# Kernel optimization log

Hardware: AMD Instinct MI355X
Metric: run time of the kernel (lower is better)

## Reference

```python
import jax, jax.numpy as jnp
import numpy as np

B, IN, N, K = 8192, 1024, 4096, 409
BN_EPS = 1e-5
BOOST_STRENGTH = 1.0


def setup_inputs() -> dict:
    key = jax.random.key(0)
    k1, k2, k3, k4, k5 = jax.random.split(key, 5)
    x = jax.random.normal(k1, (B, IN), dtype=jnp.float32)
    W = jax.random.normal(k2, (N, IN), dtype=jnp.float32) * 0.03
    b = jax.random.normal(k3, (N,), dtype=jnp.float32) * 0.01
    wmask = jax.random.randint(k4, (N, IN), 0, 2, dtype=jnp.int32)
    dutyCycle = jax.random.uniform(k5, (N,), dtype=jnp.float32) * (K / N) * 2.0
    return {"x": x, "W": W, "b": b, "wmask": wmask, "dutyCycle": dutyCycle, "k": K}


def reference(x, W, b, wmask, dutyCycle, k):
    n = W.shape[0]
    # rezeroWeights: enforce fixed weight sparsity pattern
    Wm = W * wmask.astype(W.dtype)
    # Linear
    y = jnp.einsum("bi,ni->bn", x, Wm) + b
    # BatchNorm1d(affine=False), training mode: batch mean / biased variance
    mean = jnp.mean(y, axis=0)
    var = jnp.mean(jnp.square(y - mean), axis=0)
    y = (y - mean) / jnp.sqrt(var + BN_EPS)
    # KWinners with duty-cycle boosting (k < n path)
    targetDensity = jnp.float32(k) / n
    boostFactors = jnp.exp((targetDensity - dutyCycle) * BOOST_STRENGTH)
    boosted = jax.lax.stop_gradient(y) * boostFactors  # [B, n]
    _, idx = jax.lax.top_k(boosted, k)                 # [B, k]
    rows = jnp.arange(y.shape[0])[:, None]
    out = jnp.zeros_like(y).at[rows, idx].set(jnp.take_along_axis(y, idx, axis=1))
    return out
```

## Files before the change

### kernel.cpp

```cpp
#include <hip/hip_runtime.h>

#define BATCH 8192
#define INF   1024
#define NF    4096
#define BN_EPS 1e-5
#define NT    32

typedef __attribute__((ext_vector_type(8))) short short8v;
typedef __attribute__((ext_vector_type(4))) float f32x4;

#define FENCE asm volatile("" ::: "memory")
#define BARRIER do { FENCE; __builtin_amdgcn_s_barrier(); FENCE; } while (0)

__global__ void zero_ws(double* __restrict__ p) {
    p[blockIdx.x * 256 + threadIdx.x] = 0.0;
}

__device__ __forceinline__ void split3(float x, ushort& h0, ushort& h1, ushort& h2) {
    const unsigned u0 = __float_as_uint(x) & 0xFFFF0000u;
    const float    r1 = x - __uint_as_float(u0);
    const unsigned u1 = __float_as_uint(r1) & 0xFFFF0000u;
    const float    r2 = r1 - __uint_as_float(u1);
    h0 = (ushort)(u0 >> 16);
    h1 = (ushort)(u1 >> 16);
    h2 = (ushort)(__float_as_uint(r2) >> 16);
}

__global__ __launch_bounds__(256) void split_x_kernel(
    const float* __restrict__ X, ushort* __restrict__ xs)
{
    const size_t base = ((size_t)blockIdx.x * 256 + threadIdx.x) * 8;
    const size_t LS = (size_t)BATCH * INF;
    const float4 v0 = *(const float4*)(X + base);
    const float4 v1 = *(const float4*)(X + base + 4);
    const float v[8] = {v0.x, v0.y, v0.z, v0.w, v1.x, v1.y, v1.z, v1.w};
    short8v s0, s1, s2;
#pragma unroll
    for (int i = 0; i < 8; ++i) {
        ushort h0, h1, h2;
        split3(v[i], h0, h1, h2);
        s0[i] = (short)h0; s1[i] = (short)h1; s2[i] = (short)h2;
    }
    *(short8v*)&xs[base]          = s0;
    *(short8v*)&xs[base + LS]     = s1;
    *(short8v*)&xs[base + 2 * LS] = s2;
}

__global__ __launch_bounds__(256) void split_w_kernel(
    const float* __restrict__ W, const int* __restrict__ Mk, ushort* __restrict__ wsp)
{
    const size_t base = ((size_t)blockIdx.x * 256 + threadIdx.x) * 8;
    const size_t LS = (size_t)NF * INF;
    const float4 v0 = *(const float4*)(W + base);
    const float4 v1 = *(const float4*)(W + base + 4);
    const int4   m0 = *(const int4*)(Mk + base);
    const int4   m1 = *(const int4*)(Mk + base + 4);
    const float v[8] = {v0.x * (float)m0.x, v0.y * (float)m0.y,
                        v0.z * (float)m0.z, v0.w * (float)m0.w,
                        v1.x * (float)m1.x, v1.y * (float)m1.y,
                        v1.z * (float)m1.z, v1.w * (float)m1.w};
    short8v s0, s1, s2;
#pragma unroll
    for (int i = 0; i < 8; ++i) {
        ushort h0, h1, h2;
        split3(v[i], h0, h1, h2);
        s0[i] = (short)h0; s1[i] = (short)h1; s2[i] = (short)h2;
    }
    *(short8v*)&wsp[base]          = s0;
    *(short8v*)&wsp[base + LS]     = s1;
    *(short8v*)&wsp[base + 2 * LS] = s2;
}

__device__ __forceinline__ void gload16(const ushort* g, ushort* l) {
    __builtin_amdgcn_global_load_lds(
        (const __attribute__((address_space(1))) void*)g,
        (__attribute__((address_space(3))) void*)l, 16, 0, 0);
}

__global__ __launch_bounds__(512) void gemm_mfma_fuse(
    const ushort* __restrict__ Xs, const ushort* __restrict__ Wsp,
    const float* __restrict__ bias, float* __restrict__ Y)
{
    extern __shared__ ushort sm[];
    const size_t LSX = (size_t)BATCH * INF;
    const size_t LSW = (size_t)NF * INF;

    const int t    = threadIdx.x;
    const int row0 = blockIdx.y * 128;
    const int col0 = blockIdx.x * 128;

    const int l   = t & 63;
    const int l15 = l & 15;
    const int hi  = l >> 4;
    const int wid = t >> 6;
    const int wm  = wid >> 1;
    const int wn  = wid & 1;

    const int srow  = t >> 2;
    const int sunit = (t & 3) ^ ((t >> 3) & 3);

    const int uoff = (hi ^ ((l15 >> 1) & 3)) << 3;

    f32x4  acc[2][4];
    double mst[2][4][4];
#pragma unroll
    for (int mf = 0; mf < 2; ++mf)
#pragma unroll
        for (int nf = 0; nf < 4; ++nf) {
            acc[mf][nf] = (f32x4){0.f, 0.f, 0.f, 0.f};
#pragma unroll
            for (int r = 0; r < 4; ++r) mst[mf][nf][r] = 0.0;
        }

#define PB(b, p) (sm + (b) * 24576 + (p) * 4096)

#pragma unroll
    for (int tt = 0; tt < 2; ++tt) {
#pragma unroll
        for (int p = 0; p < 3; ++p)
            gload16(Xs + (size_t)p * LSX + (size_t)(row0 + srow) * INF + tt * 32 + sunit * 8,
                    PB(tt, p) + (size_t)t * 8);
#pragma unroll
        for (int p = 0; p < 3; ++p)
            gload16(Wsp + (size_t)p * LSW + (size_t)(col0 + srow) * INF + tt * 32 + sunit * 8,
                    PB(tt, 3 + p) + (size_t)t * 8);
    }
    asm volatile("s_waitcnt vmcnt(6)" ::: "memory");
    BARRIER;

#define TILE(tt, CUR, DST) do {                                               \
    if ((tt) + 2 < NT) {                                                      \
        const int kof_ = ((tt) + 2) * 32;                                     \
        _Pragma("unroll")                                                     \
        for (int p = 0; p < 3; ++p)                                           \
            gload16(Xs + (size_t)p * LSX + (size_t)(row0 + srow) * INF + kof_ + sunit * 8, \
                    PB(DST, p) + (size_t)t * 8);                              \
        _Pragma("unroll")                                                     \
        for (int p = 0; p < 3; ++p)                                           \
            gload16(Wsp + (size_t)p * LSW + (size_t)(col0 + srow) * INF + kof_ + sunit * 8, \
                    PB(DST, 3 + p) + (size_t)t * 8);                          \
    }                                                                         \
    short8v A_[2][3], B_[4][3];                                               \
    _Pragma("unroll")                                                         \
    for (int mf = 0; mf < 2; ++mf) {                                          \
        const int ra = (wm * 32 + mf * 16 + l15) * 32 + uoff;                 \
        _Pragma("unroll")                                                     \
        for (int p = 0; p < 3; ++p)                                           \
            A_[mf][p] = *(const short8v*)&PB(CUR, p)[ra];                     \
    }                                                                         \
    _Pragma("unroll")                                                         \
    for (int nf = 0; nf < 4; ++nf) {                                          \
        const int rb = (wn * 64 + nf * 16 + l15) * 32 + uoff;                 \
        _Pragma("unroll")                                                     \
        for (int p = 0; p < 3; ++p)                                           \
            B_[nf][p] = *(const short8v*)&PB(CUR, 3 + p)[rb];                 \
    }                                                                         \
    __builtin_amdgcn_s_setprio(1);                                            \
    _Pragma("unroll")                                                         \
    for (int mf = 0; mf < 2; ++mf)                                            \
        _Pragma("unroll")                                                     \
        for (int nf = 0; nf < 4; ++nf) {                                      \
            f32x4 c = acc[mf][nf];                                            \
            c = __builtin_amdgcn_mfma_f32_16x16x32_bf16(A_[mf][0], B_[nf][0], c, 0, 0, 0); \
            c = __builtin_amdgcn_mfma_f32_16x16x32_bf16(A_[mf][0], B_[nf][1], c, 0, 0, 0); \
            c = __builtin_amdgcn_mfma_f32_16x16x32_bf16(A_[mf][1], B_[nf][0], c, 0, 0, 0); \
            c = __builtin_amdgcn_mfma_f32_16x16x32_bf16(A_[mf][0], B_[nf][2], c, 0, 0, 0); \
            c = __builtin_amdgcn_mfma_f32_16x16x32_bf16(A_[mf][1], B_[nf][1], c, 0, 0, 0); \
            c = __builtin_amdgcn_mfma_f32_16x16x32_bf16(A_[mf][2], B_[nf][0], c, 0, 0, 0); \
            acc[mf][nf] = c;                                                  \
        }                                                                     \
    __builtin_amdgcn_s_setprio(0);                                            \
    if ((tt) & 1) {                                                           \
        _Pragma("unroll")                                                     \
        for (int mf = 0; mf < 2; ++mf)                                        \
            _Pragma("unroll")                                                 \
            for (int nf = 0; nf < 4; ++nf) {                                  \
                _Pragma("unroll")                                             \
                for (int r = 0; r < 4; ++r)                                   \
                    mst[mf][nf][r] += (double)acc[mf][nf][r];                 \
                acc[mf][nf] = (f32x4){0.f, 0.f, 0.f, 0.f};                    \
            }                                                                 \
    }                                                                         \
    if ((tt) < NT - 2)       { asm volatile("s_waitcnt vmcnt(6)" ::: "memory"); } \
    else if ((tt) == NT - 2) { asm volatile("s_waitcnt vmcnt(0)" ::: "memory"); } \
    BARRIER;                                                                  \
} while (0)

    for (int tb = 0; tb + 3 <= NT; tb += 3) {
        TILE(tb,     0, 2);
        TILE(tb + 1, 1, 0);
        TILE(tb + 2, 2, 1);
    }
    TILE(30, 0, 2);
    TILE(31, 1, 0);
#undef TILE
#undef PB

#pragma unroll
    for (int mf = 0; mf < 2; ++mf)
#pragma unroll
        for (int nf = 0; nf < 4; ++nf) {
            const int colc = col0 + wn * 64 + nf * 16 + l15;
            const double bb = (double)bias[colc];
#pragma unroll
            for (int r = 0; r < 4; ++r) {
                const int roww = row0 + wm * 32 + mf * 16 + hi * 4 + r;
                Y[(size_t)roww * NF + colc] = (float)(mst[mf][nf][r] + bb);
            }
        }
}

__global__ __launch_bounds__(512) void gemm_mfma_split(
    const float* __restrict__ X, const float* __restrict__ W,
    const int* __restrict__ Mk, const float* __restrict__ bias,
    float* __restrict__ Y)
{
    __shared__ __align__(16) ushort a0s[128 * 40];
    __shared__ __align__(16) ushort a1s[128 * 40];
    __shared__ __align__(16) ushort a2s[128 * 40];
    __shared__ __align__(16) ushort b0s[128 * 40];
    __shared__ __align__(16) ushort b1s[128 * 40];
    __shared__ __align__(16) ushort b2s[128 * 40];

    const int t = threadIdx.x;
    const int row0 = blockIdx.y * 128;
    const int col0 = blockIdx.x * 128;
    const int srow = t >> 2;
    const int skb  = (t & 3) * 8;

    const float* Xp = X + (size_t)(row0 + srow) * INF + skb;
    const float* Wp = W + (size_t)(col0 + srow) * INF + skb;
    const int*   Mp = Mk + (size_t)(col0 + srow) * INF + skb;

    const int l   = t & 63;
    const int l15 = l & 15;
    const int hi  = l >> 4;
    const int wid = t >> 6;
    const int wm  = wid >> 1;
    const int wn  = wid & 1;

    f32x4  acc[2][4];
    double sh[2][4][4];
#pragma unroll
    for (int mf = 0; mf < 2; ++mf)
#pragma unroll
        for (int nf = 0; nf < 4; ++nf) {
            acc[mf][nf] = (f32x4){0.f, 0.f, 0.f, 0.f};
#pragma unroll
            for (int r = 0; r < 4; ++r) sh[mf][nf][r] = 0.0;
        }

    float4 xA0 = *(const float4*)(Xp);
    float4 xA1 = *(const float4*)(Xp + 4);
    float4 wB0 = *(const float4*)(Wp);
    float4 wB1 = *(const float4*)(Wp + 4);
    int4   mB0 = *(const int4*)(Mp);
    int4   mB1 = *(const int4*)(Mp + 4);

    for (int k0 = 0; k0 < INF; k0 += 32) {
        __syncthreads();
        {
            const float v[8] = {xA0.x, xA0.y, xA0.z, xA0.w, xA1.x, xA1.y, xA1.z, xA1.w};
            short8v s0, s1, s2;
#pragma unroll
            for (int i = 0; i < 8; ++i) {
                ushort h0, h1, h2;
                split3(v[i], h0, h1, h2);
                s0[i] = (short)h0; s1[i] = (short)h1; s2[i] = (short)h2;
            }
            const int off = srow * 40 + skb;
            *(short8v*)&a0s[off] = s0;
            *(short8v*)&a1s[off] = s1;
            *(short8v*)&a2s[off] = s2;
        }
        {
            const float wv[8] = {wB0.x * (float)mB0.x, wB0.y * (float)mB0.y,
                                 wB0.z * (float)mB0.z, wB0.w * (float)mB0.w,
                                 wB1.x * (float)mB1.x, wB1.y * (float)mB1.y,
                                 wB1.z * (float)mB1.z, wB1.w * (float)mB1.w};
            short8v s0, s1, s2;
#pragma unroll
            for (int i = 0; i < 8; ++i) {
                ushort h0, h1, h2;
                split3(wv[i], h0, h1, h2);
                s0[i] = (short)h0; s1[i] = (short)h1; s2[i] = (short)h2;
            }
            const int off = srow * 40 + skb;
            *(short8v*)&b0s[off] = s0;
            *(short8v*)&b1s[off] = s1;
            *(short8v*)&b2s[off] = s2;
        }
        __syncthreads();

        if (k0 + 32 < INF) {
            const int kn = k0 + 32;
            xA0 = *(const float4*)(Xp + kn);
            xA1 = *(const float4*)(Xp + kn + 4);
            wB0 = *(const float4*)(Wp + kn);
            wB1 = *(const float4*)(Wp + kn + 4);
            mB0 = *(const int4*)(Mp + kn);
            mB1 = *(const int4*)(Mp + kn + 4);
        }

        short8v A[2][3], B[4][3];
#pragma unroll
        for (int mf = 0; mf < 2; ++mf) {
            const int roff = (wm * 32 + mf * 16 + l15) * 40 + hi * 8;
            A[mf][0] = *(const short8v*)&a0s[roff];
            A[mf][1] = *(const short8v*)&a1s[roff];
            A[mf][2] = *(const short8v*)&a2s[roff];
        }
#pragma unroll
        for (int nf = 0; nf < 4; ++nf) {
            const int roff = (wn * 64 + nf * 16 + l15) * 40 + hi * 8;
            B[nf][0] = *(const short8v*)&b0s[roff];
            B[nf][1] = *(const short8v*)&b1s[roff];
            B[nf][2] = *(const short8v*)&b2s[roff];
        }

#pragma unroll
        for (int mf = 0; mf < 2; ++mf)
#pragma unroll
            for (int nf = 0; nf < 4; ++nf) {
                f32x4 c = acc[mf][nf];
                c = __builtin_amdgcn_mfma_f32_16x16x32_bf16(A[mf][0], B[nf][0], c, 0, 0, 0);
                c = __builtin_amdgcn_mfma_f32_16x16x32_bf16(A[mf][0], B[nf][1], c, 0, 0, 0);
                c = __builtin_amdgcn_mfma_f32_16x16x32_bf16(A[mf][1], B[nf][0], c, 0, 0, 0);
                c = __builtin_amdgcn_mfma_f32_16x16x32_bf16(A[mf][0], B[nf][2], c, 0, 0, 0);
                c = __builtin_amdgcn_mfma_f32_16x16x32_bf16(A[mf][1], B[nf][1], c, 0, 0, 0);
                c = __builtin_amdgcn_mfma_f32_16x16x32_bf16(A[mf][2], B[nf][0], c, 0, 0, 0);
                acc[mf][nf] = c;
            }

        if (k0 & 32) {
#pragma unroll
            for (int mf = 0; mf < 2; ++mf)
#pragma unroll
                for (int nf = 0; nf < 4; ++nf) {
#pragma unroll
                    for (int r = 0; r < 4; ++r) sh[mf][nf][r] += (double)acc[mf][nf][r];
                    acc[mf][nf] = (f32x4){0.f, 0.f, 0.f, 0.f};
                }
        }
    }

#pragma unroll
    for (int mf = 0; mf < 2; ++mf)
#pragma unroll
        for (int nf = 0; nf < 4; ++nf) {
            const int col = col0 + wn * 64 + nf * 16 + l15;
            const double bb = (double)bias[col];
#pragma unroll
            for (int r = 0; r < 4; ++r) {
                const int row = row0 + wm * 32 + mf * 16 + hi * 4 + r;
                Y[(size_t)row * NF + col] = (float)(sh[mf][nf][r] + bb);
            }
        }
}

__global__ __launch_bounds__(256) void stats_partial(
    const float* __restrict__ Y, double* __restrict__ dsum, double* __restrict__ dsqs)
{
    const int col = blockIdx.x * 256 + threadIdx.x;
    const int r0  = blockIdx.y * 256;
    double s = 0.0, ss = 0.0;
    for (int i = 0; i < 256; ++i) {
        const float v = Y[(size_t)(r0 + i) * NF + col];
        s  += (double)v;
        ss += (double)v * (double)v;
    }
    atomicAdd(&dsum[col], s);
    atomicAdd(&dsqs[col], ss);
}

__global__ __launch_bounds__(256) void stats_final(
    const double* __restrict__ dsum, const double* __restrict__ dsqs,
    const float* __restrict__ duty, const int* __restrict__ kp,
    double* __restrict__ mean64, double* __restrict__ rstd64, double* __restrict__ boost64,
    float* __restrict__ mean32, float* __restrict__ rstd32, float* __restrict__ boost32)
{
    const int c = blockIdx.x * 256 + threadIdx.x;
    const double m   = dsum[c] / (double)BATCH;
    const double var = dsqs[c] / (double)BATCH - m * m;
    const double rs  = 1.0 / sqrt(var + (double)BN_EPS);
    const double td  = (double)(*kp) / (double)NF;
    const double bf  = exp(td - (double)duty[c]);
    mean64[c] = m;  rstd64[c] = rs;  boost64[c] = bf;
    mean32[c] = (float)m; rstd32[c] = (float)rs; boost32[c] = (float)bf;
}

#define BAND 1e-4f
#define MAXCAND 64

__global__ __launch_bounds__(256) void topk_kernel(
    const float* __restrict__ mean32, const float* __restrict__ rstd32,
    const float* __restrict__ boost32,
    const double* __restrict__ mean64, const double* __restrict__ rstd64,
    const double* __restrict__ boost64,
    const int* __restrict__ kp,
    const float* __restrict__ X, const float* __restrict__ W,
    const int* __restrict__ Mk, const float* __restrict__ bias,
    float* __restrict__ Y)
{
    __shared__ float    yv[NF];
    __shared__ unsigned keys[NF];
    __shared__ unsigned hist[256];
    __shared__ unsigned scan[256];
    __shared__ unsigned s_bin, s_below;
    __shared__ double   red[256];
    __shared__ int      s_ncand, s_H;
    __shared__ int      cand_idx[MAXCAND];
    __shared__ double   cand_val[MAXCAND];
    __shared__ unsigned char cand_pick[MAXCAND];

    const int r = blockIdx.x;
    const int t = threadIdx.x;
    const int K = *kp;

    for (int j = 0; j < 16; ++j) {
        const int n = j * 256 + t;
        const float v   = Y[(size_t)r * NF + n];
        const float ybn = (v - mean32[n]) * rstd32[n];
        yv[n] = ybn;
        const float bst = ybn * boost32[n];
        unsigned u = __float_as_uint(bst);
        u ^= (u & 0x80000000u) ? 0xFFFFFFFFu : 0x80000000u;
        keys[n] = u;
    }
    __syncthreads();

    unsigned curval = 0u, curmask = 0u;
    int remaining = K;
    for (int pass = 3; pass >= 0; --pass) {
        const int sh = pass * 8;
        hist[t] = 0u;
        __syncthreads();
        for (int j = 0; j < 16; ++j) {
            const unsigned u = keys[j * 256 + t];
            if ((u & curmask) == curval)
                atomicAdd(&hist[(u >> sh) & 255u], 1u);
        }
        __syncthreads();
        scan[t] = hist[t];
        __syncthreads();
        for (int off = 1; off < 256; off <<= 1) {
            const unsigned add = (t + off < 256) ? scan[t + off] : 0u;
            __syncthreads();
            scan[t] += add;
            __syncthreads();
        }
        if (scan[t] >= (unsigned)remaining &&
            (t == 255 || scan[t + 1] < (unsigned)remaining)) {
            s_bin = (unsigned)t;
            s_below = (t == 255) ? 0u : scan[t + 1];
        }
        __syncthreads();
        curval |= (s_bin << sh);
        curmask |= (255u << sh);
        remaining -= (int)s_below;
        __syncthreads();
    }

    const unsigned T = curval;
    const unsigned vT = (T & 0x80000000u) ? (T ^ 0x80000000u) : ~T;
    const float cut32 = __uint_as_float(vT);
    const float cutHi = cut32 + BAND;
    const float cutLo = cut32 - BAND;

    if (t == 0) { s_ncand = 0; s_H = 0; }
    __syncthreads();
    int locH = 0;
    for (int j = 0; j < 16; ++j) {
        const int n = j * 256 + t;
        const float b = yv[n] * boost32[n];
        if (b > cutHi) {
            locH++;
        } else if (b >= cutLo) {
            const int slot = atomicAdd(&s_ncand, 1);
            if (slot < MAXCAND) cand_idx[slot] = n;
        }
    }
    atomicAdd(&s_H, locH);
    __syncthreads();
    const int H = s_H;
    const bool overflow = (s_ncand > MAXCAND);
    const int ncand = overflow ? MAXCAND : s_ncand;
    int need = K - H;
    if (need < 0) need = 0;

    if (!overflow) {
        for (int c = 0; c < ncand; ++c) {
            const int n = cand_idx[c];
            const float* xr = X + (size_t)r * INF;
            const float* wn = W + (size_t)n * INF;
            const int*   mn = Mk + (size_t)n * INF;
            double s = 0.0;
            for (int i = t; i < INF; i += 256)
                s += (double)xr[i] * (double)(wn[i] * (float)mn[i]);
            red[t] = s;
            __syncthreads();
            for (int off = 128; off > 0; off >>= 1) {
                if (t < off) red[t] += red[t + off];
                __syncthreads();
            }
            if (t == 0) {
                const double y64 = red[0] + (double)bias[n];
                cand_val[c] = (y64 - mean64[n]) * rstd64[n] * boost64[n];
                cand_pick[c] = 0;
            }
            __syncthreads();
        }
        if (t == 0) {
            for (int p = 0; p < need; ++p) {
                int best = -1;
                for (int c = 0; c < ncand; ++c) {
                    if (cand_pick[c]) continue;
                    if (best < 0 || cand_val[c] > cand_val[best] ||
                        (cand_val[c] == cand_val[best] && cand_idx[c] < cand_idx[best]))
                        best = c;
                }
                if (best < 0) break;
                cand_pick[best] = 1;
            }
        }
        __syncthreads();
        for (int j = 0; j < 16; ++j) {
            const int n = j * 256 + t;
            const float b = yv[n] * boost32[n];
            keys[n] = (b > cutHi) ? 1u : 0u;
        }
        __syncthreads();
        if (t < ncand && cand_pick[t]) keys[cand_idx[t]] = 1u;
        __syncthreads();
    } else {
        const int fneed = remaining;
        unsigned cnt = 0u;
        for (int j = 0; j < 16; ++j) cnt += (keys[t * 16 + j] == T) ? 1u : 0u;
        scan[t] = cnt;
        __syncthreads();
        for (int off = 1; off < 256; off <<= 1) {
            const unsigned add = (t >= off) ? scan[t - off] : 0u;
            __syncthreads();
            scan[t] += add;
            __syncthreads();
        }
        unsigned rank = scan[t] - cnt;
        for (int j = 0; j < 16; ++j) {
            const int n = t * 16 + j;
            const unsigned u = keys[n];
            bool sel;
            if (u == T) { sel = ((int)rank < fneed); rank++; }
            else        { sel = (u > T); }
            keys[n] = sel ? 1u : 0u;
        }
        __syncthreads();
    }

    for (int j = 0; j < 16; ++j) {
        const int n = j * 256 + t;
        Y[(size_t)r * NF + n] = keys[n] ? yv[n] : 0.0f;
    }
}

extern "C" void kernel_launch(void* const* d_in, const int* in_sizes, int n_in,
                              void* d_out, int out_size, void* d_ws, size_t ws_size,
                              hipStream_t stream)
{
    const float* x     = (const float*)d_in[0];
    const float* W     = (const float*)d_in[1];
    const float* b     = (const float*)d_in[2];
    const int*   wmask = (const int*)d_in[3];
    const float* duty  = (const float*)d_in[4];
    const int*   kp    = (const int*)d_in[5];
    float* out = (float*)d_out;

    const size_t SPLIT_X_ELTS = (size_t)3 * BATCH * INF;
    const size_t SPLIT_W_ELTS = (size_t)3 * NF * INF;
    const size_t STATS_BYTES  = (size_t)5 * NF * sizeof(double) + (size_t)3 * NF * sizeof(float);
    const size_t NEED_FAST    = (SPLIT_X_ELTS + SPLIT_W_ELTS) * sizeof(ushort) + STATS_BYTES;
    const bool fast = (ws_size >= NEED_FAST);

    ushort* xs  = (ushort*)d_ws;
    ushort* wsp = xs + SPLIT_X_ELTS;
    char* statbase = fast ? (char*)(wsp + SPLIT_W_ELTS) : (char*)d_ws;

    double* dsum    = (double*)statbase;
    double* dsqs    = dsum + NF;
    double* mean64  = dsqs + NF;
    double* rstd64  = mean64 + NF;
    double* boost64 = rstd64 + NF;
    float*  mean32  = (float*)(boost64 + NF);
    float*  rstd32  = mean32 + NF;
    float*  boost32 = rstd32 + NF;

    hipLaunchKernelGGL(zero_ws, dim3(2 * NF / 256), dim3(256), 0, stream, dsum);

    if (fast) {
        hipLaunchKernelGGL(split_x_kernel, dim3(BATCH * INF / 8 / 256), dim3(256), 0, stream,
                           x, xs);
        hipLaunchKernelGGL(split_w_kernel, dim3(NF * INF / 8 / 256), dim3(256), 0, stream,
                           W, wmask, wsp);
        hipFuncSetAttribute((const void*)gemm_mfma_fuse,
                            hipFuncAttributeMaxDynamicSharedMemorySize, 147456);
        hipLaunchKernelGGL(gemm_mfma_fuse, dim3(NF / 128, BATCH / 128), dim3(512), 147456,
                           stream, xs, wsp, b, out);
    } else {
        hipLaunchKernelGGL(gemm_mfma_split, dim3(NF / 128, BATCH / 128), dim3(512), 0, stream,
                           x, W, wmask, b, out);
    }

    hipLaunchKernelGGL(stats_partial, dim3(NF / 256, BATCH / 256), dim3(256), 0, stream,
                       out, dsum, dsqs);
    hipLaunchKernelGGL(stats_final, dim3(NF / 256), dim3(256), 0, stream,
                       dsum, dsqs, duty, kp,
                       mean64, rstd64, boost64, mean32, rstd32, boost32);
    hipLaunchKernelGGL(topk_kernel, dim3(BATCH), dim3(256), 0, stream,
                       mean32, rstd32, boost32, mean64, rstd64, boost64, kp,
                       x, W, wmask, b, out);
}
```

Before: 570.1 us.

## Fuse BN column statistics into GEMM epilogue and speed up top-k radix select

The GEMM epilogue now accumulates per-column sums and squared sums in double precision, reduces them through shared memory, and atomically adds them to global buffers. This removes the separate stats_partial pass, which reread the full output matrix. The top-k kernel gains vectorized float4 loads and stores, a wave-shuffle suffix scan in place of the barrier-heavy Hillis-Steele scan, and compaction of the first-pass bin into a small list so later radix passes scan fewer keys. The trade-off is double atomics per block and a fallback path when the selected bin overflows the list.

After: 558.3 us. 2.1% less time.

```diff
diff --git a/kernel.cpp b/kernel.cpp
--- a/kernel.cpp
+++ b/kernel.cpp
@@ -79,7 +79,8 @@
 
 __global__ __launch_bounds__(512) void gemm_mfma_fuse(
     const ushort* __restrict__ Xs, const ushort* __restrict__ Wsp,
-    const float* __restrict__ bias, float* __restrict__ Y)
+    const float* __restrict__ bias, float* __restrict__ Y,
+    double* __restrict__ dsum, double* __restrict__ dsqs)
 {
     extern __shared__ ushort sm[];
     const size_t LSX = (size_t)BATCH * INF;
@@ -98,7 +99,6 @@
 
     const int srow  = t >> 2;
     const int sunit = (t & 3) ^ ((t >> 3) & 3);
-
     const int uoff = (hi ^ ((l15 >> 1) & 3)) << 3;
 
     f32x4  acc[2][4];
@@ -196,18 +196,41 @@
 #undef TILE
 #undef PB
 
-#pragma unroll
-    for (int mf = 0; mf < 2; ++mf)
-#pragma unroll
-        for (int nf = 0; nf < 4; ++nf) {
-            const int colc = col0 + wn * 64 + nf * 16 + l15;
-            const double bb = (double)bias[colc];
+    double* sdsum = (double*)sm;
+    double* sdsqs = sdsum + 16 * 128;
+    const int grp = wm * 4 + hi;
+#pragma unroll
+    for (int nf = 0; nf < 4; ++nf) {
+        const int colL = wn * 64 + nf * 16 + l15;
+        const int colc = col0 + colL;
+        const double bb = (double)bias[colc];
+        double s = 0.0, q = 0.0;
+#pragma unroll
+        for (int mf = 0; mf < 2; ++mf)
 #pragma unroll
             for (int r = 0; r < 4; ++r) {
                 const int roww = row0 + wm * 32 + mf * 16 + hi * 4 + r;
-                Y[(size_t)roww * NF + colc] = (float)(mst[mf][nf][r] + bb);
-            }
-        }
+                const float yval = (float)(mst[mf][nf][r] + bb);
+                Y[(size_t)roww * NF + colc] = yval;
+                s += (double)yval;
+                q += (double)yval * (double)yval;
+            }
+        sdsum[grp * 128 + colL] = s;
+        sdsqs[grp * 128 + colL] = q;
+    }
+    __syncthreads();
+    if (t < 128) {
+        double s = 0.0;
+#pragma unroll
+        for (int g = 0; g < 16; ++g) s += sdsum[g * 128 + t];
+        atomicAdd(&dsum[col0 + t], s);
+    } else if (t < 256) {
+        const int c = t - 128;
+        double q = 0.0;
+#pragma unroll
+        for (int g = 0; g < 16; ++g) q += sdsqs[g * 128 + c];
+        atomicAdd(&dsqs[col0 + c], q);
+    }
 }
 
 __global__ __launch_bounds__(512) void gemm_mfma_split(
@@ -391,6 +414,7 @@
 
 #define BAND 1e-4f
 #define MAXCAND 64
+#define LCAP 512
 
 __global__ __launch_bounds__(256) void topk_kernel(
     const float* __restrict__ mean32, const float* __restrict__ rstd32,
@@ -406,7 +430,10 @@
     __shared__ unsigned keys[NF];
     __shared__ unsigned hist[256];
     __shared__ unsigned scan[256];
+    __shared__ unsigned wtot[4];
     __shared__ unsigned s_bin, s_below;
+    __shared__ int      s_cnt;
+    __shared__ unsigned lkey[LCAP];
     __shared__ double   red[256];
     __shared__ int      s_ncand, s_H;
     __shared__ int      cand_idx[MAXCAND];
@@ -416,39 +443,93 @@
     const int r = blockIdx.x;
     const int t = threadIdx.x;
     const int K = *kp;
+    const int lane = t & 63;
+    const int w    = t >> 6;
+
+    for (int j = 0; j < 4; ++j) {
+        const int n = j * 1024 + t * 4;
+        const float4 v  = *(const float4*)&Y[(size_t)r * NF + n];
+        const float4 mm = *(const float4*)&mean32[n];
+        const float4 rs = *(const float4*)&rstd32[n];
+        const float4 bo = *(const float4*)&boost32[n];
+        const float yb[4] = {(v.x - mm.x) * rs.x, (v.y - mm.y) * rs.y,
+                             (v.z - mm.z) * rs.z, (v.w - mm.w) * rs.w};
+        const float bsv[4] = {yb[0] * bo.x, yb[1] * bo.y, yb[2] * bo.z, yb[3] * bo.w};
+#pragma unroll
+        for (int q = 0; q < 4; ++q) {
+            yv[n + q] = yb[q];
+            unsigned u = __float_as_uint(bsv[q]);
+            u ^= (u & 0x80000000u) ? 0xFFFFFFFFu : 0x80000000u;
+            keys[n + q] = u;
+        }
+    }
+    __syncthreads();
+
+#define SUFFIX_SCAN() do {                                                    \
+    unsigned v_ = hist[t];                                                    \
+    _Pragma("unroll")                                                         \
+    for (int off_ = 1; off_ < 64; off_ <<= 1) {                               \
+        const unsigned o_ = __shfl_down(v_, off_, 64);                        \
+        if (lane + off_ < 64) v_ += o_;                                       \
+    }                                                                         \
+    if (lane == 0) wtot[w] = v_;                                              \
+    __syncthreads();                                                          \
+    unsigned add_ = 0;                                                        \
+    for (int ww_ = w + 1; ww_ < 4; ++ww_) add_ += wtot[ww_];                  \
+    scan[t] = v_ + add_;                                                      \
+    __syncthreads();                                                          \
+} while (0)
+
+    hist[t] = 0u;
+    __syncthreads();
+    for (int j = 0; j < 16; ++j)
+        atomicAdd(&hist[keys[j * 256 + t] >> 24], 1u);
+    __syncthreads();
+    SUFFIX_SCAN();
+    int remaining = K;
+    if (scan[t] >= (unsigned)remaining &&
+        (t == 255 || scan[t + 1] < (unsigned)remaining)) {
+        s_bin = (unsigned)t;
+        s_below = (t == 255) ? 0u : scan[t + 1];
+    }
+    if (t == 0) s_cnt = 0;
+    __syncthreads();
+    const unsigned b1 = s_bin;
+    unsigned curval = b1 << 24;
+    unsigned curmask = 0xFF000000u;
+    remaining -= (int)s_below;
+    __syncthreads();
 
     for (int j = 0; j < 16; ++j) {
-        const int n = j * 256 + t;
-        const float v   = Y[(size_t)r * NF + n];
-        const float ybn = (v - mean32[n]) * rstd32[n];
-        yv[n] = ybn;
-        const float bst = ybn * boost32[n];
-        unsigned u = __float_as_uint(bst);
-        u ^= (u & 0x80000000u) ? 0xFFFFFFFFu : 0x80000000u;
-        keys[n] = u;
-    }
-    __syncthreads();
-
-    unsigned curval = 0u, curmask = 0u;
-    int remaining = K;
-    for (int pass = 3; pass >= 0; --pass) {
+        const unsigned u = keys[j * 256 + t];
+        if ((u >> 24) == b1) {
+            const int slot = atomicAdd(&s_cnt, 1);
+            if (slot < LCAP) lkey[slot] = u;
+        }
+    }
+    __syncthreads();
+    const bool smallbin = (s_cnt <= LCAP);
+    const int cnt = s_cnt;
+
+    for (int pass = 2; pass >= 0; --pass) {
         const int sh = pass * 8;
         hist[t] = 0u;
         __syncthreads();
-        for (int j = 0; j < 16; ++j) {
-            const unsigned u = keys[j * 256 + t];
-            if ((u & curmask) == curval)
-                atomicAdd(&hist[(u >> sh) & 255u], 1u);
-        }
-        __syncthreads();
-        scan[t] = hist[t];
-        __syncthreads();
-        for (int off = 1; off < 256; off <<= 1) {
-            const unsigned add = (t + off < 256) ? scan[t + off] : 0u;
-            __syncthreads();
-            scan[t] += add;
-            __syncthreads();
-        }
+        if (smallbin) {
+            for (int i = t; i < cnt; i += 256) {
+                const unsigned u = lkey[i];
+                if ((u & curmask) == curval)
+                    atomicAdd(&hist[(u >> sh) & 255u], 1u);
+            }
+        } else {
+            for (int j = 0; j < 16; ++j) {
+                const unsigned u = keys[j * 256 + t];
+                if ((u & curmask) == curval)
+                    atomicAdd(&hist[(u >> sh) & 255u], 1u);
+            }
+        }
+        __syncthreads();
+        SUFFIX_SCAN();
         if (scan[t] >= (unsigned)remaining &&
             (t == 255 || scan[t + 1] < (unsigned)remaining)) {
             s_bin = (unsigned)t;
@@ -460,6 +541,7 @@
         remaining -= (int)s_below;
         __syncthreads();
     }
+#undef SUFFIX_SCAN
 
     const unsigned T = curval;
     const unsigned vT = (T & 0x80000000u) ? (T ^ 0x80000000u) : ~T;
@@ -534,9 +616,9 @@
         __syncthreads();
     } else {
         const int fneed = remaining;
-        unsigned cnt = 0u;
-        for (int j = 0; j < 16; ++j) cnt += (keys[t * 16 + j] == T) ? 1u : 0u;
-        scan[t] = cnt;
+        unsigned cntk = 0u;
+        for (int j = 0; j < 16; ++j) cntk += (keys[t * 16 + j] == T) ? 1u : 0u;
+        scan[t] = cntk;
         __syncthreads();
         for (int off = 1; off < 256; off <<= 1) {
             const unsigned add = (t >= off) ? scan[t - off] : 0u;
@@ -544,7 +626,7 @@
             scan[t] += add;
             __syncthreads();
         }
-        unsigned rank = scan[t] - cnt;
+        unsigned rank = scan[t] - cntk;
         for (int j = 0; j < 16; ++j) {
             const int n = t * 16 + j;
             const unsigned u = keys[n];
@@ -556,9 +638,14 @@
         __syncthreads();
     }
 
-    for (int j = 0; j < 16; ++j) {
-        const int n = j * 256 + t;
-        Y[(size_t)r * NF + n] = keys[n] ? yv[n] : 0.0f;
+    for (int j = 0; j < 4; ++j) {
+        const int n = j * 1024 + t * 4;
+        float4 o;
+        o.x = keys[n + 0] ? yv[n + 0] : 0.0f;
+        o.y = keys[n + 1] ? yv[n + 1] : 0.0f;
+        o.z = keys[n + 2] ? yv[n + 2] : 0.0f;
+        o.w = keys[n + 3] ? yv[n + 3] : 0.0f;
+        *(float4*)&Y[(size_t)r * NF + n] = o;
     }
 }
 
@@ -603,14 +690,14 @@
         hipFuncSetAttribute((const void*)gemm_mfma_fuse,
                             hipFuncAttributeMaxDynamicSharedMemorySize, 147456);
         hipLaunchKernelGGL(gemm_mfma_fuse, dim3(NF / 128, BATCH / 128), dim3(512), 147456,
-                           stream, xs, wsp, b, out);
+                           stream, xs, wsp, b, out, dsum, dsqs);
     } else {
         hipLaunchKernelGGL(gemm_mfma_split, dim3(NF / 128, BATCH / 128), dim3(512), 0, stream,
                            x, W, wmask, b, out);
-    }
-
-    hipLaunchKernelGGL(stats_partial, dim3(NF / 256, BATCH / 256), dim3(256), 0, stream,
-                       out, dsum, dsqs);
+        hipLaunchKernelGGL(stats_partial, dim3(NF / 256, BATCH / 256), dim3(256), 0, stream,
+                           out, dsum, dsqs);
+    }
+
     hipLaunchKernelGGL(stats_final, dim3(NF / 256), dim3(256), 0, stream,
                        dsum, dsqs, duty, kp,
                        mean64, rstd64, boost64, mean32, rstd32, boost32);
```
